# Kernel optimization log

Measured on AMD Instinct MI355X. Metric: run time of the kernel, lower is better.

Reference implementation:

```python
import jax, jax.numpy as jnp
import numpy as np
from jax.scipy.linalg import expm

B, S, D = 8, 2048, 1024          # batch, seq, input_dim
C, CD = 16, 64                   # num_concepts, concept_dim
L = C * CD                       # latent_dim = 1024
ALPHA, BETA = 0.3, 1.0
LN_EPS = 1e-5                    # torch nn.LayerNorm default


def layer_norm(x, g, b):
    m = jnp.mean(x, axis=-1, keepdims=True)
    v = jnp.mean(jnp.square(x - m), axis=-1, keepdims=True)
    return (x - m) * jax.lax.rsqrt(v + LN_EPS) * g + b


def setup_inputs() -> dict:
    key = jax.random.key(0)
    ks = jax.random.split(key, 8)
    sc = 0.02
    return {
        "x": jax.random.normal(ks[0], (B, S, D), jnp.float32),
        # encoder: Linear(D, 2L) + LayerNorm(2L)
        "enc_w": jax.random.normal(ks[1], (2 * L, D), jnp.float32) * sc,
        "enc_b": jnp.zeros((2 * L,), jnp.float32),
        "enc_g": jnp.ones((2 * L,), jnp.float32),
        "enc_bt": jnp.zeros((2 * L,), jnp.float32),
        # DAG weights [C, C] (torch inits zeros; use small random for non-trivial math)
        "dag_w": jax.random.normal(ks[2], (C, C), jnp.float32) * 0.1,
        # per-concept transforms: Linear(CD,CD) -> LN(CD) -> ReLU -> Linear(CD,CD), stacked over C
        "cw1": jax.random.normal(ks[3], (C, CD, CD), jnp.float32) * sc,
        "cb1": jnp.zeros((C, CD), jnp.float32),
        "cg": jnp.ones((C, CD), jnp.float32),
        "cbt": jnp.zeros((C, CD), jnp.float32),
        "cw2": jax.random.normal(ks[4], (C, CD, CD), jnp.float32) * sc,
        "cb2": jnp.zeros((C, CD), jnp.float32),
        # decoder: Linear(L,L) -> LN(L) -> ReLU -> Linear(L,D)
        "dec_w1": jax.random.normal(ks[5], (L, L), jnp.float32) * sc,
        "dec_b1": jnp.zeros((L,), jnp.float32),
        "dec_g": jnp.ones((L,), jnp.float32),
        "dec_bt": jnp.zeros((L,), jnp.float32),
        "dec_w2": jax.random.normal(ks[6], (D, L), jnp.float32) * sc,
        "dec_b2": jnp.zeros((D,), jnp.float32),
    }


def reference(x, enc_w, enc_b, enc_g, enc_bt, dag_w, cw1, cb1, cg, cbt, cw2, cb2,
              dec_w1, dec_b1, dec_g, dec_bt, dec_w2, dec_b2):
    # ---- encode ----
    h = layer_norm(jnp.einsum('bsd,kd->bsk', x, enc_w) + enc_b, enc_g, enc_bt)  # [B,S,2L]
    mu, logvar = jnp.split(h, 2, axis=-1)                                        # [B,S,L] each
    z = mu  # eval-mode reparameterize

    # ---- causal transform ----
    zc = z.reshape(B, S, C, CD)                                   # [B,S,C,CD]
    dag = jnp.tril(jax.nn.softplus(dag_w), k=-1)                  # [C,C]
    z_causal = zc + jnp.einsum('ij,bsjd->bsid', dag, zc)          # [B,S,C,CD]

    # per-concept Linear -> LN -> ReLU -> Linear, batched over concept axis
    t = jnp.einsum('bsce,cde->bscd', z_causal, cw1) + cb1         # [B,S,C,CD]
    t = layer_norm(t, cg, cbt)
    t = jax.nn.relu(t)
    t = jnp.einsum('bsce,cde->bscd', t, cw2) + cb2
    z_t = t.reshape(B, S, L)

    # ---- decode ----
    d = layer_norm(jnp.einsum('bsl,kl->bsk', z_t, dec_w1) + dec_b1, dec_g, dec_bt)
    d = jax.nn.relu(d)
    x_recon = jnp.einsum('bsl,dl->bsd', d, dec_w2) + dec_b2        # [B,S,D]

    # ---- losses ----
    recon_loss = jnp.mean(jnp.square(x_recon - x))
    kl_loss = -0.5 * jnp.mean(1.0 + logvar - jnp.square(mu) - jnp.exp(logvar))
    dag_loss = jnp.sum(jnp.abs(dag)) + jnp.trace(expm(dag))
    total_loss = recon_loss + ALPHA * kl_loss + BETA * dag_loss
    return x_recon, total_loss, kl_loss, recon_loss, dag_loss
```

## Files before the change

kernel.cpp:

```cpp
#include <hip/hip_runtime.h>
#include <stdint.h>


#define NTOK   16384
#define DIM    1024
#define NC     16
#define CD     64
#define NOUT_ELEMS 16777216

typedef float f32x4 __attribute__((ext_vector_type(4)));
typedef __bf16 bf16x8 __attribute__((ext_vector_type(8)));
typedef unsigned short u16x4 __attribute__((ext_vector_type(4)));
typedef unsigned short u16x8 __attribute__((ext_vector_type(8)));

__device__ float g_scal[3];
__device__ float g_part[512];

__device__ __forceinline__ float b2f(uint16_t u) {
  union { uint32_t i; float f; } v; v.i = ((uint32_t)u) << 16; return v.f;
}
__device__ __forceinline__ uint16_t f2b(float f) {
  union { float f; uint32_t i; } v; v.f = f;
  uint32_t x = v.i;
  return (uint16_t)((x + 0x7fffu + ((x >> 16) & 1u)) >> 16);
}

__device__ __forceinline__ void gload_lds16(const uint16_t* g, uint16_t* l) {
  __builtin_amdgcn_global_load_lds(
      (const __attribute__((address_space(1))) void*)g,
      (__attribute__((address_space(3))) void*)l, 16, 0, 0);
}

__device__ __forceinline__ void cvt8(const float* s, uint16_t* d) {
  const f32x4 a = *(const f32x4*)s;
  const f32x4 b = *(const f32x4*)(s + 4);
  u16x8 o;
  o[0]=f2b(a[0]); o[1]=f2b(a[1]); o[2]=f2b(a[2]); o[3]=f2b(a[3]);
  o[4]=f2b(b[0]); o[5]=f2b(b[1]); o[6]=f2b(b[2]); o[7]=f2b(b[3]);
  *(u16x8*)d = o;
}

__global__ __launch_bounds__(256) void cvt_x_kernel(
    const float* __restrict__ src, uint16_t* __restrict__ dst)
{
  const int i = blockIdx.x * 256 + threadIdx.x;
  cvt8(src + (size_t)i * 8, dst + (size_t)i * 8);
}

__global__ __launch_bounds__(256) void cvt_weights_kernel(
    const float* __restrict__ ew, const float* __restrict__ d1,
    const float* __restrict__ d2, const float* __restrict__ c1,
    const float* __restrict__ c2, uint16_t* __restrict__ out)
{
  const int i = blockIdx.x * 256 + threadIdx.x;
  const float* src; uint16_t* dst; int off;
  if (i < 262144)      { src = ew; dst = out;           off = i; }
  else if (i < 393216) { src = d1; dst = out + 2097152; off = i - 262144; }
  else if (i < 524288) { src = d2; dst = out + 3145728; off = i - 393216; }
  else if (i < 532480) { src = c1; dst = out + 4194304; off = i - 524288; }
  else                 { src = c2; dst = out + 4259840; off = i - 532480; }
  cvt8(src + (size_t)off * 8, dst + (size_t)off * 8);
}

__device__ __forceinline__ void stage_half(
    const uint16_t* __restrict__ G, uint16_t* L, int h, int lda,
    int sr, int pc, int wave)
{
#pragma unroll
  for (int i = 0; i < 2; ++i) {
    const int r = h * 128 + i * 64 + sr;
    gload_lds16(G + (size_t)r * lda + (size_t)((pc ^ (sr & 7)) * 8),
                (uint16_t*)((char*)L + h * 16384 + i * 8192 + wave * 1024));
  }
}

template<typename TC, bool SPLIT, bool RECON>
__global__ __launch_bounds__(512, 2) void gemm256_kernel(
    const uint16_t* __restrict__ A, const uint16_t* __restrict__ Wm,
    const float* __restrict__ bias, TC* __restrict__ C0, TC* __restrict__ C1,
    const float* __restrict__ Xref,
    int K, int lda, int ldw, int ldc)
{
  __shared__ __align__(16) uint16_t lds[65536];

  const int tid  = threadIdx.x;
  const int wave = tid >> 6;
  const int lane = tid & 63;
  const int q    = lane >> 4;
  const int r16  = lane & 15;
  const int wm   = wave >> 2;
  const int wn   = wave & 3;
  const int sr   = tid >> 3;
  const int pc   = tid & 7;

  const int gx  = gridDim.x;
  const int gy  = gridDim.y;
  const int nwg = gx * gy;
  const int o   = blockIdx.y * gx + blockIdx.x;
  const int w   = (o & 7) * (nwg >> 3) + (o >> 3);
  const int bn  = (w & (gy - 1)) * 256;
  const int bm  = (w >> __builtin_ctz(gy)) * 256;

  const uint16_t* Ab = A  + (size_t)bm * lda;
  const uint16_t* Wb = Wm + (size_t)bn * ldw;

  const int T = K >> 6;

  stage_half(Ab,      lds,                 0, lda, sr, pc, wave);
  stage_half(Ab,      lds,                 1, lda, sr, pc, wave);
  stage_half(Wb,      lds + 16384,         0, ldw, sr, pc, wave);
  stage_half(Wb,      lds + 16384,         1, ldw, sr, pc, wave);
  if (T > 1) {
    stage_half(Wb + 64, lds + 32768 + 16384, 0, ldw, sr, pc, wave);
    stage_half(Wb + 64, lds + 32768 + 16384, 1, ldw, sr, pc, wave);
    asm volatile("s_waitcnt vmcnt(4)" ::: "memory");
  } else {
    asm volatile("s_waitcnt vmcnt(0)" ::: "memory");
  }
  __builtin_amdgcn_s_barrier();

  f32x4 acc[8][4] = {};
  const int cxa = r16 & 7;
  const int c0  = (q ^ cxa) * 8;
  const int c1  = ((4 + q) ^ cxa) * 8;

  for (int t = 0; t < T; ++t) {
    uint16_t* As  = lds + (t & 1) * 32768;
    uint16_t* Bs  = As + 16384;
    uint16_t* Asn = lds + ((t & 1) ^ 1) * 32768;

    const uint16_t* a_rd = As + (wm * 128 + r16) * 64;
    const uint16_t* b_rd = Bs + (wn * 64  + r16) * 64;

    bf16x8 bfr[4][2];

#pragma unroll
    for (int p = 0; p < 4; ++p) {
      bf16x8 af[2][2];
#pragma unroll
      for (int mi2 = 0; mi2 < 2; ++mi2) {
        af[mi2][0] = *(const bf16x8*)(a_rd + (p * 2 + mi2) * 1024 + c0);
        af[mi2][1] = *(const bf16x8*)(a_rd + (p * 2 + mi2) * 1024 + c1);
      }
      if (p == 0) {
#pragma unroll
        for (int ni = 0; ni < 4; ++ni) {
          bfr[ni][0] = *(const bf16x8*)(b_rd + ni * 1024 + c0);
          bfr[ni][1] = *(const bf16x8*)(b_rd + ni * 1024 + c1);
        }
        if (t + 1 < T) {
          stage_half(Ab + (size_t)(t + 1) * 64, Asn, 0, lda, sr, pc, wave);
          stage_half(Ab + (size_t)(t + 1) * 64, Asn, 1, lda, sr, pc, wave);
        }
      } else if (p == 1) {
        if (t + 2 < T)
          stage_half(Wb + (size_t)(t + 2) * 64, Bs, 0, ldw, sr, pc, wave);
      } else if (p == 2) {
        if (t + 2 < T)
          stage_half(Wb + (size_t)(t + 2) * 64, Bs, 1, ldw, sr, pc, wave);
      }

      __builtin_amdgcn_s_barrier();
      __builtin_amdgcn_s_setprio(1);
#pragma unroll
      for (int ks = 0; ks < 2; ++ks)
#pragma unroll
        for (int mi2 = 0; mi2 < 2; ++mi2)
#pragma unroll
          for (int ni = 0; ni < 4; ++ni)
            acc[p * 2 + mi2][ni] = __builtin_amdgcn_mfma_f32_16x16x32_bf16(
                af[mi2][ks], bfr[ni][ks], acc[p * 2 + mi2][ni], 0, 0, 0);
      __builtin_amdgcn_s_setprio(0);
      if (p == 3) {
        if (t + 2 < T)      asm volatile("s_waitcnt vmcnt(4)" ::: "memory");
        else if (t + 1 < T) asm volatile("s_waitcnt vmcnt(0)" ::: "memory");
      }
      __builtin_amdgcn_s_barrier();
    }
  }

  TC* Cq = C0;
  int cb = bn;
  if constexpr (SPLIT) {
    if (bn >= 1024) { Cq = C1; cb = bn - 1024; }
  }
  float bv[4];
#pragma unroll
  for (int ni = 0; ni < 4; ++ni) bv[ni] = bias[bn + wn * 64 + ni * 16 + r16];

  float rsum = 0.f;
#pragma unroll
  for (int mi = 0; mi < 8; ++mi) {
    const int rbase = bm + wm * 128 + mi * 16 + q * 4;
#pragma unroll
    for (int r = 0; r < 4; ++r) {
      const size_t rowoff = (size_t)(rbase + r) * ldc + cb;
#pragma unroll
      for (int ni = 0; ni < 4; ++ni) {
        const int loc = wn * 64 + ni * 16 + r16;
        const float v = acc[mi][ni][r] + bv[ni];
        if constexpr (sizeof(TC) == 2)
          Cq[rowoff + loc] = f2b(v);
        else
          Cq[rowoff + loc] = v;
        if constexpr (RECON) {
          const float dd = v - Xref[rowoff + loc];
          rsum += dd * dd;
        }
      }
    }
  }
  if constexpr (RECON) {
#pragma unroll
    for (int m = 1; m < 64; m <<= 1) rsum += __shfl_xor(rsum, m);
    __shared__ float redR[8];
    if (lane == 0) redR[wave] = rsum;
    __syncthreads();
    if (tid == 0) {
      float s = 0.f;
#pragma unroll
      for (int w2 = 0; w2 < 8; ++w2) s += redR[w2];
      atomicAdd(&g_part[256 + (w & 255)], s);
    }
  }
}

__global__ __launch_bounds__(256) void concept_fused_kernel(
    uint16_t* __restrict__ z, const uint16_t* __restrict__ c1b,
    const uint16_t* __restrict__ c2b, const float* __restrict__ cb1,
    const float* __restrict__ cg, const float* __restrict__ cbt,
    const float* __restrict__ cb2)
{
  __shared__ __align__(16) uint16_t Az[128 * 64];
  __shared__ __align__(16) uint16_t W1s[64 * 64];
  __shared__ __align__(16) uint16_t W2s[64 * 64];

  const int tid  = threadIdx.x;
  const int wave = tid >> 6;
  const int lane = tid & 63;
  const int q    = lane >> 4;
  const int r16  = lane & 15;
  const int c    = blockIdx.y;
  const int m0   = blockIdx.x * 128;

  const int lr = tid >> 3;
  const int pc = tid & 7;

#pragma unroll
  for (int i = 0; i < 4; ++i) {
    const int r = i * 32 + lr;
    const int gc = pc ^ (r & 7);
    gload_lds16(z + (size_t)(m0 + r) * DIM + c * 64 + gc * 8,
                (uint16_t*)((char*)Az + i * 4096 + wave * 1024));
  }
#pragma unroll
  for (int i = 0; i < 2; ++i) {
    const int r = i * 32 + lr;
    const int gc = pc ^ (r & 7);
    gload_lds16(c1b + (size_t)c * 4096 + r * 64 + gc * 8,
                (uint16_t*)((char*)W1s + i * 4096 + wave * 1024));
    gload_lds16(c2b + (size_t)c * 4096 + r * 64 + gc * 8,
                (uint16_t*)((char*)W2s + i * 4096 + wave * 1024));
  }
  __syncthreads();

  f32x4 acc[2][4] = {};
#pragma unroll
  for (int ks = 0; ks < 2; ++ks) {
    bf16x8 af[2], wf[4];
#pragma unroll
    for (int mi = 0; mi < 2; ++mi) {
      const int row = wave * 32 + mi * 16 + r16;
      af[mi] = *(const bf16x8*)(Az + row * 64 + ((ks * 4 + q) ^ (row & 7)) * 8);
    }
#pragma unroll
    for (int ni = 0; ni < 4; ++ni) {
      const int d = ni * 16 + r16;
      wf[ni] = *(const bf16x8*)(W1s + d * 64 + ((ks * 4 + q) ^ (d & 7)) * 8);
    }
#pragma unroll
    for (int mi = 0; mi < 2; ++mi)
#pragma unroll
      for (int ni = 0; ni < 4; ++ni)
        acc[mi][ni] = __builtin_amdgcn_mfma_f32_16x16x32_bf16(
            af[mi], wf[ni], acc[mi][ni], 0, 0, 0);
  }

  float b1v[4], cgv[4], cbv[4], b2v[4];
#pragma unroll
  for (int ni = 0; ni < 4; ++ni) {
    const int cn = ni * 16 + r16;
    b1v[ni] = cb1[c * 64 + cn];
    cgv[ni] = cg[c * 64 + cn];
    cbv[ni] = cbt[c * 64 + cn];
    b2v[ni] = cb2[c * 64 + cn];
  }
#pragma unroll
  for (int mi = 0; mi < 2; ++mi) {
#pragma unroll
    for (int r = 0; r < 4; ++r) {
      float s1 = 0.f, s2 = 0.f;
#pragma unroll
      for (int ni = 0; ni < 4; ++ni) {
        const float v = acc[mi][ni][r] + b1v[ni];
        acc[mi][ni][r] = v;
        s1 += v; s2 += v * v;
      }
#pragma unroll
      for (int m = 1; m < 16; m <<= 1) {
        s1 += __shfl_xor(s1, m);
        s2 += __shfl_xor(s2, m);
      }
      const float mean = s1 * (1.f / 64.f);
      const float var  = s2 * (1.f / 64.f) - mean * mean;
      const float rs   = rsqrtf(var + 1e-5f);
      const int row = wave * 32 + mi * 16 + q * 4 + r;
#pragma unroll
      for (int ni = 0; ni < 4; ++ni) {
        const float y = fmaxf((acc[mi][ni][r] - mean) * rs * cgv[ni] + cbv[ni], 0.f);
        const int cn = ni * 16 + r16;
        Az[row * 64 + (((cn >> 3) ^ (row & 7)) * 8) + (cn & 7)] = f2b(y);
      }
    }
  }
  __syncthreads();

  f32x4 acc2[2][4] = {};
#pragma unroll
  for (int ks = 0; ks < 2; ++ks) {
    bf16x8 af[2], wf[4];
#pragma unroll
    for (int mi = 0; mi < 2; ++mi) {
      const int row = wave * 32 + mi * 16 + r16;
      af[mi] = *(const bf16x8*)(Az + row * 64 + ((ks * 4 + q) ^ (row & 7)) * 8);
    }
#pragma unroll
    for (int ni = 0; ni < 4; ++ni) {
      const int d = ni * 16 + r16;
      wf[ni] = *(const bf16x8*)(W2s + d * 64 + ((ks * 4 + q) ^ (d & 7)) * 8);
    }
#pragma unroll
    for (int mi = 0; mi < 2; ++mi)
#pragma unroll
      for (int ni = 0; ni < 4; ++ni)
        acc2[mi][ni] = __builtin_amdgcn_mfma_f32_16x16x32_bf16(
            af[mi], wf[ni], acc2[mi][ni], 0, 0, 0);
  }

#pragma unroll
  for (int mi = 0; mi < 2; ++mi)
#pragma unroll
    for (int ni = 0; ni < 4; ++ni) {
      const int cn = ni * 16 + r16;
#pragma unroll
      for (int r = 0; r < 4; ++r) {
        const int row = wave * 32 + mi * 16 + q * 4 + r;
        z[(size_t)(m0 + row) * DIM + c * 64 + cn] = f2b(acc2[mi][ni][r] + b2v[ni]);
      }
    }
}

__global__ __launch_bounds__(256) void kl_causal_kernel(
    const uint16_t* __restrict__ lv, uint16_t* __restrict__ mu,
    const float* __restrict__ g, const float* __restrict__ b,
    const float* __restrict__ dag_w)
{
  __shared__ __align__(16) float zsh[1024];
  __shared__ float dg[256];
  __shared__ float red[8];
  __shared__ float red2[4];
  const int tid = threadIdx.x;
  const int tok = blockIdx.x;
  const int e0  = tid * 4;

  {
    const int di = tid >> 4, dj = tid & 15;
    dg[tid] = (dj < di) ? log1pf(expf(dag_w[tid])) : 0.f;
  }

  const uint16_t* lvp = lv + (size_t)tok * 1024;
  uint16_t*       mup = mu + (size_t)tok * 1024;

  const u16x4 m4 = *(const u16x4*)(mup + e0);
  const u16x4 l4 = *(const u16x4*)(lvp + e0);
  float xm[4], xl[4];
  float s1 = 0.f, s2 = 0.f;
#pragma unroll
  for (int k = 0; k < 4; ++k) {
    xm[k] = b2f(m4[k]);
    xl[k] = b2f(l4[k]);
    s1 += xm[k] + xl[k];
    s2 += xm[k] * xm[k] + xl[k] * xl[k];
  }
#pragma unroll
  for (int m = 1; m < 64; m <<= 1) {
    s1 += __shfl_xor(s1, m);
    s2 += __shfl_xor(s2, m);
  }
  const int wave = tid >> 6, lane = tid & 63;
  if (lane == 0) { red[wave] = s1; red[4 + wave] = s2; }
  __syncthreads();
  s1 = red[0] + red[1] + red[2] + red[3];
  s2 = red[4] + red[5] + red[6] + red[7];
  const float mean = s1 * (1.f / 2048.f);
  const float var  = s2 * (1.f / 2048.f) - mean * mean;
  const float rs   = rsqrtf(var + 1e-5f);

  const f32x4 g4m = *(const f32x4*)(g + e0);
  const f32x4 b4m = *(const f32x4*)(b + e0);
  const f32x4 g4l = *(const f32x4*)(g + 1024 + e0);
  const f32x4 b4l = *(const f32x4*)(b + 1024 + e0);
  float kl = 0.f;
  f32x4 z;
#pragma unroll
  for (int k = 0; k < 4; ++k) {
    z[k] = (xm[k] - mean) * rs * g4m[k] + b4m[k];
    const float y = (xl[k] - mean) * rs * g4l[k] + b4l[k];
    kl += 1.f + y - z[k] * z[k] - expf(y);
  }
  *(f32x4*)(zsh + e0) = z;
#pragma unroll
  for (int m = 1; m < 64; m <<= 1) kl += __shfl_xor(kl, m);
  if (lane == 0) red2[wave] = kl;
  __syncthreads();
  if (tid == 0)
    atomicAdd(&g_part[tok & 255], red2[0] + red2[1] + red2[2] + red2[3]);

  const int i  = e0 >> 6;
  const int d0 = e0 & 63;
  f32x4 s = *(const f32x4*)(zsh + e0);
  for (int j = 0; j < i; ++j) {
    const float w = dg[i * 16 + j];
    const f32x4 zj = *(const f32x4*)(zsh + j * 64 + d0);
    s[0] += w * zj[0]; s[1] += w * zj[1]; s[2] += w * zj[2]; s[3] += w * zj[3];
  }
  u16x4 o;
#pragma unroll
  for (int k = 0; k < 4; ++k) o[k] = f2b(s[k]);
  *(u16x4*)(mup + e0) = o;
}

__global__ __launch_bounds__(256) void ln_relu_kernel(
    uint16_t* __restrict__ data, const float* __restrict__ g,
    const float* __restrict__ b)
{
  const int tid = threadIdx.x;
  const int e0  = tid * 4;
  uint16_t* p = data + (size_t)blockIdx.x * 1024;

  const u16x4 v4 = *(const u16x4*)(p + e0);
  float x[4];
  float s1 = 0.f, s2 = 0.f;
#pragma unroll
  for (int k = 0; k < 4; ++k) {
    x[k] = b2f(v4[k]);
    s1 += x[k];
    s2 += x[k] * x[k];
  }
#pragma unroll
  for (int m = 1; m < 64; m <<= 1) {
    s1 += __shfl_xor(s1, m);
    s2 += __shfl_xor(s2, m);
  }
  __shared__ float red[8];
  const int wave = tid >> 6, lane = tid & 63;
  if (lane == 0) { red[wave] = s1; red[4 + wave] = s2; }
  __syncthreads();
  s1 = red[0] + red[1] + red[2] + red[3];
  s2 = red[4] + red[5] + red[6] + red[7];
  const float mean = s1 * (1.f / 1024.f);
  const float var  = s2 * (1.f / 1024.f) - mean * mean;
  const float rs   = rsqrtf(var + 1e-5f);

  const f32x4 g4 = *(const f32x4*)(g + e0);
  const f32x4 b4 = *(const f32x4*)(b + e0);
  u16x4 o;
#pragma unroll
  for (int k = 0; k < 4; ++k) {
    const float y = (x[k] - mean) * rs * g4[k] + b4[k];
    o[k] = f2b(fmaxf(y, 0.f));
  }
  *(u16x4*)(p + e0) = o;
}

__global__ __launch_bounds__(256) void dag_init_kernel(
    const float* __restrict__ dag_w)
{
  const int t = threadIdx.x;
  g_part[t] = 0.f;
  g_part[256 + t] = 0.f;
  const int i = t >> 4, j = t & 15;
  const float v = (j < i) ? log1pf(expf(dag_w[t])) : 0.f;
  float s = v;
#pragma unroll
  for (int m = 1; m < 64; m <<= 1) s += __shfl_xor(s, m);
  __shared__ float red[4];
  const int wave = t >> 6, lane = t & 63;
  if (lane == 0) red[wave] = s;
  __syncthreads();
  if (t == 0)
    g_scal[2] = red[0] + red[1] + red[2] + red[3] + 16.f;
}

__global__ __launch_bounds__(256) void finalize_kernel(float* __restrict__ out_tail)
{
  const int tid = threadIdx.x;
  float kl = g_part[tid];
  float rc = g_part[256 + tid];
#pragma unroll
  for (int m = 1; m < 64; m <<= 1) {
    kl += __shfl_xor(kl, m);
    rc += __shfl_xor(rc, m);
  }
  __shared__ float red[8];
  const int wave = tid >> 6, lane = tid & 63;
  if (lane == 0) { red[wave] = kl; red[4 + wave] = rc; }
  __syncthreads();
  if (tid == 0) {
    const float kls = red[0] + red[1] + red[2] + red[3];
    const float rcs = red[4] + red[5] + red[6] + red[7];
    const float kl_l   = -0.5f * kls * (1.f / (16384.f * 1024.f));
    const float recon  = rcs * (1.f / 16777216.f);
    const float dagl   = g_scal[2];
    out_tail[0] = recon + 0.3f * kl_l + 1.0f * dagl;
    out_tail[1] = kl_l;
    out_tail[2] = recon;
    out_tail[3] = dagl;
  }
}

extern "C" void kernel_launch(void* const* d_in, const int* in_sizes, int n_in,
                              void* d_out, int out_size, void* d_ws, size_t ws_size,
                              hipStream_t stream) {
  const float* x      = (const float*)d_in[0];
  const float* enc_w  = (const float*)d_in[1];
  const float* enc_b  = (const float*)d_in[2];
  const float* enc_g  = (const float*)d_in[3];
  const float* enc_bt = (const float*)d_in[4];
  const float* dag_w  = (const float*)d_in[5];
  const float* cw1    = (const float*)d_in[6];
  const float* cb1    = (const float*)d_in[7];
  const float* cg     = (const float*)d_in[8];
  const float* cbt    = (const float*)d_in[9];
  const float* cw2    = (const float*)d_in[10];
  const float* cb2    = (const float*)d_in[11];
  const float* dec_w1 = (const float*)d_in[12];
  const float* dec_b1 = (const float*)d_in[13];
  const float* dec_g  = (const float*)d_in[14];
  const float* dec_bt = (const float*)d_in[15];
  const float* dec_w2 = (const float*)d_in[16];
  const float* dec_b2 = (const float*)d_in[17];

  uint16_t* S    = (uint16_t*)d_ws;
  uint16_t* Wbf  = (uint16_t*)((char*)d_ws + (size_t)NTOK * DIM * 2);
  uint16_t* ewb  = Wbf;
  uint16_t* d1b  = Wbf + 2097152;
  uint16_t* d2b  = Wbf + 3145728;
  uint16_t* c1b  = Wbf + 4194304;
  uint16_t* c2b  = Wbf + 4259840;

  uint16_t* Obf  = (uint16_t*)d_out;
  uint16_t* xbf  = Obf + (size_t)NOUT_ELEMS;
  float*    O    = (float*)d_out;

  dag_init_kernel<<<1, 256, 0, stream>>>(dag_w);

  cvt_x_kernel<<<NOUT_ELEMS / 8 / 256, 256, 0, stream>>>(x, xbf);
  cvt_weights_kernel<<<2112, 256, 0, stream>>>(enc_w, dec_w1, dec_w2, cw1, cw2, Wbf);

  gemm256_kernel<uint16_t, true, false>
      <<<dim3(64, 8, 1), 512, 0, stream>>>(
      xbf, ewb, enc_b, Obf, S, nullptr, DIM, DIM, DIM, DIM);

  kl_causal_kernel<<<NTOK, 256, 0, stream>>>(S, Obf, enc_g, enc_bt, dag_w);

  concept_fused_kernel<<<dim3(128, 16, 1), 256, 0, stream>>>(
      Obf, c1b, c2b, cb1, cg, cbt, cb2);

  gemm256_kernel<uint16_t, false, false>
      <<<dim3(64, 4, 1), 512, 0, stream>>>(
      Obf, d1b, dec_b1, S, S, nullptr, DIM, DIM, DIM, DIM);

  ln_relu_kernel<<<NTOK, 256, 0, stream>>>(S, dec_g, dec_bt);

  gemm256_kernel<float, false, true>
      <<<dim3(64, 4, 1), 512, 0, stream>>>(
      S, d2b, dec_b2, O, O, x, DIM, DIM, DIM, DIM);

  finalize_kernel<<<1, 256, 0, stream>>>(O + (size_t)NOUT_ELEMS);
}
```

Before: 376.7 us.

## Restructure GEMM k-loop to two barriers per tile with register-prefetched A fragments

New measurement: 383.0 us. No clear change (+1.7%).

```diff
diff --git a/kernel.cpp b/kernel.cpp
--- a/kernel.cpp
+++ b/kernel.cpp
@@ -132,51 +132,61 @@
     const uint16_t* a_rd = As + (wm * 128 + r16) * 64;
     const uint16_t* b_rd = Bs + (wn * 64  + r16) * 64;
 
-    bf16x8 bfr[4][2];
-
-#pragma unroll
-    for (int p = 0; p < 4; ++p) {
-      bf16x8 af[2][2];
-#pragma unroll
-      for (int mi2 = 0; mi2 < 2; ++mi2) {
-        af[mi2][0] = *(const bf16x8*)(a_rd + (p * 2 + mi2) * 1024 + c0);
-        af[mi2][1] = *(const bf16x8*)(a_rd + (p * 2 + mi2) * 1024 + c1);
+    bf16x8 bfr[4][2], af0[2][2];
+#pragma unroll
+    for (int ni = 0; ni < 4; ++ni) {
+      bfr[ni][0] = *(const bf16x8*)(b_rd + ni * 1024 + c0);
+      bfr[ni][1] = *(const bf16x8*)(b_rd + ni * 1024 + c1);
+    }
+#pragma unroll
+    for (int mi2 = 0; mi2 < 2; ++mi2) {
+      af0[mi2][0] = *(const bf16x8*)(a_rd + mi2 * 1024 + c0);
+      af0[mi2][1] = *(const bf16x8*)(a_rd + mi2 * 1024 + c1);
+    }
+    if (t + 1 < T) {
+      stage_half(Ab + (size_t)(t + 1) * 64, Asn, 0, lda, sr, pc, wave);
+      stage_half(Ab + (size_t)(t + 1) * 64, Asn, 1, lda, sr, pc, wave);
+    }
+    asm volatile("s_waitcnt lgkmcnt(0)" ::: "memory");
+    __builtin_amdgcn_s_barrier();
+    if (t + 2 < T) {
+      stage_half(Wb + (size_t)(t + 2) * 64, Bs, 0, ldw, sr, pc, wave);
+      stage_half(Wb + (size_t)(t + 2) * 64, Bs, 1, ldw, sr, pc, wave);
+    }
+
+    __builtin_amdgcn_s_setprio(1);
+#pragma unroll
+    for (int ks = 0; ks < 2; ++ks)
+#pragma unroll
+      for (int mi2 = 0; mi2 < 2; ++mi2)
+#pragma unroll
+        for (int ni = 0; ni < 4; ++ni)
+          acc[mi2][ni] = __builtin_amdgcn_mfma_f32_16x16x32_bf16(
+              af0[mi2][ks], bfr[ni][ks], acc[mi2][ni], 0, 0, 0);
+
+    bf16x8 aP0 = *(const bf16x8*)(a_rd + 2 * 1024 + c0);
+    bf16x8 aP1 = *(const bf16x8*)(a_rd + 2 * 1024 + c1);
+#pragma unroll
+    for (int mi = 2; mi < 8; ++mi) {
+      const bf16x8 a0 = aP0, a1 = aP1;
+      if (mi < 7) {
+        aP0 = *(const bf16x8*)(a_rd + (mi + 1) * 1024 + c0);
+        aP1 = *(const bf16x8*)(a_rd + (mi + 1) * 1024 + c1);
       }
-      if (p == 0) {
-#pragma unroll
-        for (int ni = 0; ni < 4; ++ni) {
-          bfr[ni][0] = *(const bf16x8*)(b_rd + ni * 1024 + c0);
-          bfr[ni][1] = *(const bf16x8*)(b_rd + ni * 1024 + c1);
-        }
-        if (t + 1 < T) {
-          stage_half(Ab + (size_t)(t + 1) * 64, Asn, 0, lda, sr, pc, wave);
-          stage_half(Ab + (size_t)(t + 1) * 64, Asn, 1, lda, sr, pc, wave);
-        }
-      } else if (p == 1) {
-        if (t + 2 < T)
-          stage_half(Wb + (size_t)(t + 2) * 64, Bs, 0, ldw, sr, pc, wave);
-      } else if (p == 2) {
-        if (t + 2 < T)
-          stage_half(Wb + (size_t)(t + 2) * 64, Bs, 1, ldw, sr, pc, wave);
-      }
-
-      __builtin_amdgcn_s_barrier();
-      __builtin_amdgcn_s_setprio(1);
-#pragma unroll
-      for (int ks = 0; ks < 2; ++ks)
-#pragma unroll
-        for (int mi2 = 0; mi2 < 2; ++mi2)
-#pragma unroll
-          for (int ni = 0; ni < 4; ++ni)
-            acc[p * 2 + mi2][ni] = __builtin_amdgcn_mfma_f32_16x16x32_bf16(
-                af[mi2][ks], bfr[ni][ks], acc[p * 2 + mi2][ni], 0, 0, 0);
-      __builtin_amdgcn_s_setprio(0);
-      if (p == 3) {
-        if (t + 2 < T)      asm volatile("s_waitcnt vmcnt(4)" ::: "memory");
-        else if (t + 1 < T) asm volatile("s_waitcnt vmcnt(0)" ::: "memory");
-      }
-      __builtin_amdgcn_s_barrier();
-    }
+#pragma unroll
+      for (int ni = 0; ni < 4; ++ni)
+        acc[mi][ni] = __builtin_amdgcn_mfma_f32_16x16x32_bf16(
+            a0, bfr[ni][0], acc[mi][ni], 0, 0, 0);
+#pragma unroll
+      for (int ni = 0; ni < 4; ++ni)
+        acc[mi][ni] = __builtin_amdgcn_mfma_f32_16x16x32_bf16(
+            a1, bfr[ni][1], acc[mi][ni], 0, 0, 0);
+    }
+    __builtin_amdgcn_s_setprio(0);
+
+    if (t + 2 < T)      asm volatile("s_waitcnt vmcnt(4)" ::: "memory");
+    else if (t + 1 < T) asm volatile("s_waitcnt vmcnt(0)" ::: "memory");
+    __builtin_amdgcn_s_barrier();
   }
 
   TC* Cq = C0;
```
